# Kernel optimization log

Measured on AMD Instinct MI355X. Metric: run time of the kernel, lower is better.

The kernel has to match this reference:

```python
import jax, jax.numpy as jnp
import numpy as np

N_NODES = 20000
IN_C = 512
OUT_C = 128
HEADS = 4
N_EDGES = 320000
NEG_SLOPE = 0.2


def setup_inputs() -> dict:
    key = jax.random.key(0)
    ks = jax.random.split(key, 10)
    x = jax.random.normal(ks[0], (N_NODES, IN_C), dtype=jnp.float32)
    edge_index = jax.random.randint(ks[1], (2, N_EDGES), 0, N_NODES, dtype=jnp.int64)
    s = 0.05
    return {
        "x": x,
        "edge_index": edge_index,
        "W1": jax.random.normal(ks[2], (IN_C, HEADS * OUT_C), dtype=jnp.float32) * s,
        "a_src1": jax.random.normal(ks[3], (HEADS, OUT_C), dtype=jnp.float32) * s,
        "a_dst1": jax.random.normal(ks[4], (HEADS, OUT_C), dtype=jnp.float32) * s,
        "b1": jnp.zeros((HEADS * OUT_C,), dtype=jnp.float32),
        "W2": jax.random.normal(ks[5], (HEADS * OUT_C, 1 * OUT_C), dtype=jnp.float32) * s,
        "a_src2": jax.random.normal(ks[6], (1, OUT_C), dtype=jnp.float32) * s,
        "a_dst2": jax.random.normal(ks[7], (1, OUT_C), dtype=jnp.float32) * s,
        "b2": jnp.zeros((OUT_C,), dtype=jnp.float32),
    }


def gat_conv(x, src, dst, W, a_src, a_dst, b, heads, out_c, concat):
    N = x.shape[0]
    h = (x @ W).reshape(N, heads, out_c)            # [N,H,C]
    al_src = jnp.sum(h * a_src, axis=-1)            # [N,H]
    al_dst = jnp.sum(h * a_dst, axis=-1)            # [N,H]
    e = jax.nn.leaky_relu(al_src[src] + al_dst[dst], NEG_SLOPE)  # [E,H]
    # segment softmax over edges grouped by destination node
    e_max = jax.ops.segment_max(e, dst, num_segments=N)         # [N,H]
    e = jnp.exp(e - e_max[dst])
    denom = jax.ops.segment_sum(e, dst, num_segments=N)         # [N,H]
    alpha = e / (denom[dst] + 1e-16)                             # [E,H]
    msg = h[src] * alpha[:, :, None]                             # [E,H,C]
    out = jax.ops.segment_sum(msg, dst, num_segments=N)          # [N,H,C]
    out = out.reshape(N, heads * out_c) if concat else jnp.mean(out, axis=1)
    return out + b


def reference(x, edge_index, W1, a_src1, a_dst1, b1, W2, a_src2, a_dst2, b2):
    N = x.shape[0]
    # PyG GATConv adds self-loops by default
    loops = jnp.arange(N, dtype=edge_index.dtype)
    src = jnp.concatenate([edge_index[0], loops])
    dst = jnp.concatenate([edge_index[1], loops])
    h = gat_conv(x, src, dst, W1, a_src1, a_dst1, b1, HEADS, OUT_C, concat=True)
    h = jax.nn.elu(h)
    return gat_conv(h, src, dst, W2, a_src2, a_dst2, b2, 1, OUT_C, concat=False)
```

## Files before the change

kernel.cpp:

```cpp
#include <hip/hip_runtime.h>
#include <hip/hip_bf16.h>

typedef __hip_bfloat16 bf16;
typedef __bf16 bf16x8 __attribute__((ext_vector_type(8)));
typedef float f32x4 __attribute__((ext_vector_type(4)));

#define NEG_SLOPE 0.2f
#define F32_THRESH 256


__device__ __forceinline__ bool is_f32(const int* fcnt) { return *fcnt > F32_THRESH; }

__device__ __forceinline__ float ld_f(const void* p, long long i, bool f32) {
    return f32 ? ((const float*)p)[i] : __bfloat162float(((const bf16*)p)[i]);
}

__device__ __forceinline__ float b2f(unsigned hs) {
    return __uint_as_float(hs << 16);
}

__device__ __forceinline__ void load_lds16(const void* g, void* l) {
    __builtin_amdgcn_global_load_lds(
        (const __attribute__((address_space(1))) void*)g,
        (__attribute__((address_space(3))) void*)l, 16, 0, 0);
}

__global__ void k_sniff(const unsigned* w, long long nw, int* cnt) {
    int c = 0;
    for (long long i = blockIdx.x * (long long)blockDim.x + threadIdx.x; i < nw;
         i += (long long)gridDim.x * blockDim.x)
        if ((w[i] & 0x7F80u) == 0x7F80u) c++;
    if (c) atomicAdd(cnt, c);
}

__global__ void k_tobf16(const void* src, const int* fcnt, bf16* dst,
                         long long n_valid, long long n_total) {
    bool f32 = is_f32(fcnt);
    for (long long i = blockIdx.x * (long long)blockDim.x + threadIdx.x; i < n_total;
         i += (long long)gridDim.x * blockDim.x)
        dst[i] = (i < n_valid) ? __float2bfloat16(ld_f(src, i, f32))
                               : __float2bfloat16(0.f);
}


__global__ void k_detect_i32(const int* idx, int n_half, int* iflag) {
    int any = 0;
    for (int i = blockIdx.x * blockDim.x + threadIdx.x; i < n_half;
         i += gridDim.x * blockDim.x)
        if (idx[2 * i + 1] != 0) any = 1;
    if (any) atomicOr(iflag, 1);
}

__device__ __forceinline__ int edge_val(const void* idx, long long i, int is64) {
    return is64 ? (int)((const long long*)idx)[i] : ((const int*)idx)[i];
}


__global__ void k_count(const void* idx, const int* iflag, int E0, int N, int* deg) {
    int e = blockIdx.x * blockDim.x + threadIdx.x;
    if (e >= E0 + N) return;
    int is64 = (*iflag == 0);
    int d = (e < E0) ? edge_val(idx, (long long)E0 + e, is64) : (e - E0);
    if ((unsigned)d >= (unsigned)N) d = 0;
    atomicAdd(&deg[d], 1);
}

__global__ __launch_bounds__(1024) void k_scan(const int* deg, int* rowptr, int N) {
    __shared__ int part[1024];
    int t = threadIdx.x;
    int chunk = (N + 1023) / 1024;
    int s = t * chunk, e = min(N, s + chunk);
    int sum = 0;
    for (int i = s; i < e; i++) sum += deg[i];
    part[t] = sum;
    __syncthreads();
    for (int off = 1; off < 1024; off <<= 1) {
        int v = (t >= off) ? part[t - off] : 0;
        __syncthreads();
        part[t] += v;
        __syncthreads();
    }
    int run = (t == 0) ? 0 : part[t - 1];
    for (int i = s; i < e; i++) { rowptr[i] = run; run += deg[i]; }
    if (t == 1023) rowptr[N] = part[1023];
}

__global__ void k_scatter(const void* idx, const int* iflag, int E0, int N,
                          const int* rowptr, int* cursor, int* csr_src) {
    int e = blockIdx.x * blockDim.x + threadIdx.x;
    if (e >= E0 + N) return;
    int is64 = (*iflag == 0);
    int s, d;
    if (e < E0) {
        s = edge_val(idx, e, is64);
        d = edge_val(idx, (long long)E0 + e, is64);
    } else {
        s = d = e - E0;
    }
    if ((unsigned)s >= (unsigned)N) s = 0;
    if ((unsigned)d >= (unsigned)N) d = 0;
    int pos = rowptr[d] + atomicAdd(&cursor[d], 1);
    if ((unsigned)pos < (unsigned)(E0 + N)) csr_src[pos] = s;
}


__global__ void k_transpose(const void* W, const int* fcnt, bf16* Wt, int K, int N) {
    int i = blockIdx.x * blockDim.x + threadIdx.x;
    if (i >= K * N) return;
    bool f32 = is_f32(fcnt);
    int k = i / N, n = i % N;
    Wt[(size_t)n * K + k] = __float2bfloat16(ld_f(W, i, f32));
}


__global__ void k_al(const bf16* __restrict__ h, const void* a_s, const void* a_d,
                     const int* fcnt, float* als, float* ald, int N, int H) {
    __shared__ float sa[512], sd[512];
    const int HC = H * 128;
    bool f32 = is_f32(fcnt);
    for (int i = threadIdx.x; i < HC; i += blockDim.x) {
        sa[i] = ld_f(a_s, i, f32);
        sd[i] = ld_f(a_d, i, f32);
    }
    __syncthreads();
    int i = blockIdx.x * blockDim.x + threadIdx.x;
    if (i >= N * H) return;
    int n = i / H, hh = i % H;
    const uint4* row = (const uint4*)(h + (size_t)n * HC + hh * 128);
    float s = 0.f, d = 0.f;
#pragma unroll
    for (int q = 0; q < 16; q++) {
        uint4 u = row[q];
        unsigned uu[4] = {u.x, u.y, u.z, u.w};
#pragma unroll
        for (int t = 0; t < 4; t++) {
            float v0 = b2f(uu[t] & 0xFFFFu), v1 = b2f(uu[t] >> 16);
            int c = hh * 128 + q * 8 + t * 2;
            s += v0 * sa[c] + v1 * sa[c + 1];
            d += v0 * sd[c] + v1 * sd[c + 1];
        }
    }
    als[i] = s;
    ald[i] = d;
}


template <int BN>
__global__ __launch_bounds__(256) void k_gemm(const bf16* __restrict__ A,
                                              const bf16* __restrict__ Bt,
                                              bf16* __restrict__ C,
                                              int M, int Nn, int K) {
    constexpr int BM = 128, BK = 32;
    constexpr int NT = BN / 32;
    const int m0 = blockIdx.x * BM;
    const int n0 = blockIdx.y * BN;
    __shared__ __bf16 As[BM][BK];
    __shared__ __bf16 Bs[BN][BK];
    const int tid = threadIdx.x;
    const int wave = tid >> 6;
    const int lane = tid & 63;
    const int wm = (wave & 1) * 64;
    const int wn = (wave >> 1) * (NT * 16);
    const int lm = lane & 15;
    const int quad = lane >> 4;
    const int srow = tid >> 2;
    const int scol = (tid & 3) * 8;

    f32x4 acc[4][NT];
#pragma unroll
    for (int mt = 0; mt < 4; mt++)
#pragma unroll
        for (int nt = 0; nt < NT; nt++) acc[mt][nt] = (f32x4){0.f, 0.f, 0.f, 0.f};

    const char* Ab = (const char*)(A + (size_t)(m0 + srow) * K + scol);
    const char* Bb = (const char*)(Bt + (size_t)(n0 + srow) * K + scol);
    char* ldsA = (char*)&As[0][0] + wave * 1024;
    char* ldsB = (char*)&Bs[0][0] + wave * 1024;
    const size_t rstep = (size_t)64 * K * 2;

    for (int k0 = 0; k0 < K; k0 += BK) {
        __syncthreads();
        const size_t kb = (size_t)k0 * 2;
        load_lds16(Ab + kb, ldsA);
        load_lds16(Ab + kb + rstep, ldsA + 4096);
        load_lds16(Bb + kb, ldsB);
        if (BN == 128) load_lds16(Bb + kb + rstep, ldsB + 4096);
        __syncthreads();
        bf16x8 af[4], bfv[NT];
#pragma unroll
        for (int mt = 0; mt < 4; mt++)
            af[mt] = *(const bf16x8*)&As[wm + mt * 16 + lm][quad * 8];
#pragma unroll
        for (int nt = 0; nt < NT; nt++)
            bfv[nt] = *(const bf16x8*)&Bs[wn + nt * 16 + lm][quad * 8];
#pragma unroll
        for (int mt = 0; mt < 4; mt++)
#pragma unroll
            for (int nt = 0; nt < NT; nt++)
                acc[mt][nt] = __builtin_amdgcn_mfma_f32_16x16x32_bf16(
                    af[mt], bfv[nt], acc[mt][nt], 0, 0, 0);
    }

#pragma unroll
    for (int mt = 0; mt < 4; mt++) {
        int rb = m0 + wm + mt * 16 + quad * 4;
#pragma unroll
        for (int nt = 0; nt < NT; nt++) {
            int col = n0 + wn + nt * 16 + lm;
#pragma unroll
            for (int r = 0; r < 4; r++) {
                int row = rb + r;
                if (row < M) C[(size_t)row * Nn + col] = __float2bfloat16(acc[mt][nt][r]);
            }
        }
    }
}


template <int C, int H, bool ELU, bool DYN_OUT, int BS>
__global__ __launch_bounds__(BS) void k_agg(
    const bf16* __restrict__ feat, const float* __restrict__ als,
    const float* __restrict__ ald, const int* __restrict__ rowptr,
    const int* __restrict__ csr_src, const void* bias, const int* fcnt,
    void* outp, int N, int E) {
    constexpr int NW = BS / 64;
    constexpr int CPL = C / 64;
    constexpr int Ch = C / H;
    constexpr int OPT = C / BS;
    const int n = blockIdx.x;
    const int tid = threadIdx.x;
    const int wave = tid >> 6;
    const int lane = tid & 63;
    const int c0 = lane * CPL;
    const int head = c0 / Ch;

    __shared__ float red[NW][C];
    __shared__ float ps[NW][H];

    int start = rowptr[n];
    if (start < 0) start = 0;
    int end = rowptr[n + 1];
    if (end > E) end = E;
    int deg = end - start;
    if (deg < 0) deg = 0;

    float aldn[H];
#pragma unroll
    for (int h = 0; h < H; h++) aldn[h] = ald[(size_t)n * H + h];

    float acc[CPL] = {};
    float psum[H] = {};

#pragma unroll 2
    for (int e = wave; e < deg; e += NW) {
        int s = csr_src[start + e];
        if ((unsigned)s >= (unsigned)N) s = 0;
        float w[H];
        if (H == 4) {
            float4 av = ((const float4*)als)[s];
            float a4[4] = {av.x, av.y, av.z, av.w};
#pragma unroll
            for (int h = 0; h < 4; h++) {
                float l = a4[h] + aldn[h];
                l = l > 0.f ? l : NEG_SLOPE * l;
                w[h] = __expf(fminf(l, 60.f));
                psum[h] += w[h];
            }
        } else {
            float l = als[s] + aldn[0];
            l = l > 0.f ? l : NEG_SLOPE * l;
            w[0] = __expf(fminf(l, 60.f));
            psum[0] += w[0];
        }
        float wl;
        if (H == 1) wl = w[0];
        else wl = head < 2 ? (head == 0 ? w[0] : w[1]) : (head == 2 ? w[2] : w[3]);

        const bf16* fr = feat + (size_t)s * C + c0;
        if (CPL == 8) {
            uint4 u = *(const uint4*)fr;
            unsigned uu[4] = {u.x, u.y, u.z, u.w};
#pragma unroll
            for (int q = 0; q < 4; q++) {
                acc[2 * q] += wl * b2f(uu[q] & 0xFFFFu);
                acc[2 * q + 1] += wl * b2f(uu[q] >> 16);
            }
        } else {
            unsigned u = *(const unsigned*)fr;
            acc[0] += wl * b2f(u & 0xFFFFu);
            acc[1] += wl * b2f(u >> 16);
        }
    }

#pragma unroll
    for (int j = 0; j < CPL; j++) red[wave][c0 + j] = acc[j];
    if (lane == 0)
#pragma unroll
        for (int h = 0; h < H; h++) ps[wave][h] = psum[h];
    __syncthreads();

    const bool f32 = is_f32(fcnt);
#pragma unroll
    for (int p = 0; p < OPT; p++) {
        int c = tid * OPT + p;
        int h = c / Ch;
        float sv = 0.f;
#pragma unroll
        for (int w2 = 0; w2 < NW; w2++) sv += red[w2][c];
        float dn = 1e-16f;
#pragma unroll
        for (int w2 = 0; w2 < NW; w2++) dn += ps[w2][h];
        float v = sv / dn + ld_f(bias, c, f32);
        if (ELU) v = v > 0.f ? v : expf(v) - 1.f;
        size_t oi = (size_t)n * C + c;
        if (DYN_OUT && f32) ((float*)outp)[oi] = v;
        else ((bf16*)outp)[oi] = __float2bfloat16(v);
    }
}


extern "C" void kernel_launch(void* const* d_in, const int* in_sizes, int n_in,
                              void* d_out, int out_size, void* d_ws, size_t ws_size,
                              hipStream_t stream) {
    const int N = in_sizes[0] / 512;
    const int K = 512;
    const int C1 = 512;
    const int C2 = 128;
    const int H1 = 4;
    const int E0 = in_sizes[1] / 2;
    const int E = E0 + N;
    const int Mpad = (N + 127) / 128 * 128;

    const void* x_raw = d_in[0];
    const void* eidx = d_in[1];
    const void* W1 = d_in[2];
    const void* as1 = d_in[3];
    const void* ad1 = d_in[4];
    const void* b1 = d_in[5];
    const void* W2 = d_in[6];
    const void* as2 = d_in[7];
    const void* ad2 = d_in[8];
    const void* b2 = d_in[9];

    char* ws = (char*)d_ws;
    size_t off = 0;
    auto take = [&](size_t bytes) {
        size_t r = off;
        off += (bytes + 255) & ~(size_t)255;
        return r;
    };
    bf16* xb     = (bf16*)(ws + take((size_t)Mpad * K * 2));
    bf16* h1     = (bf16*)(ws + take((size_t)N * C1 * 2));
    bf16* hagg   = (bf16*)(ws + take((size_t)Mpad * C1 * 2));
    bf16* W1t    = (bf16*)(ws + take((size_t)K * C1 * 2));
    bf16* W2t    = (bf16*)(ws + take((size_t)C1 * C2 * 2));
    float* al1s  = (float*)(ws + take((size_t)N * H1 * 4));
    float* al1d  = (float*)(ws + take((size_t)N * H1 * 4));
    int* rowptr  = (int*)(ws + take((size_t)(N + 1) * 4));
    int* csr_src = (int*)(ws + take((size_t)E * 4));
    int* deg     = (int*)(ws + take((size_t)(2 * N + 2) * 4));
    int* cursor  = deg + N;
    int* iflag   = deg + 2 * N;
    int* fcnt    = deg + 2 * N + 1;
    bf16* h2     = xb;
    float* al2s  = al1s;
    float* al2d  = al1d;
    if (off > ws_size) return;

    hipMemsetAsync(deg, 0, (size_t)(2 * N + 2) * 4, stream);
    hipMemsetAsync(csr_src, 0, (size_t)E * 4, stream);

    long long nw = (long long)in_sizes[0] / 2;
    if (nw > (1 << 20)) nw = 1 << 20;
    k_sniff<<<256, 256, 0, stream>>>((const unsigned*)x_raw, nw, fcnt);
    int nh = E0 > (1 << 16) ? (1 << 16) : E0;
    k_detect_i32<<<64, 256, 0, stream>>>((const int*)eidx, nh, iflag);

    k_count<<<(E + 255) / 256, 256, 0, stream>>>(eidx, iflag, E0, N, deg);
    k_scan<<<1, 1024, 0, stream>>>(deg, rowptr, N);
    k_scatter<<<(E + 255) / 256, 256, 0, stream>>>(eidx, iflag, E0, N, rowptr, cursor, csr_src);

    k_tobf16<<<2048, 256, 0, stream>>>(x_raw, fcnt, xb, (long long)N * K, (long long)Mpad * K);
    k_transpose<<<(K * C1 + 255) / 256, 256, 0, stream>>>(W1, fcnt, W1t, K, C1);
    k_transpose<<<(C1 * C2 + 255) / 256, 256, 0, stream>>>(W2, fcnt, W2t, C1, C2);

    dim3 g1(Mpad / 128, C1 / 128);
    k_gemm<128><<<g1, 256, 0, stream>>>(xb, W1t, h1, N, C1, K);
    k_al<<<(N * H1 + 255) / 256, 256, 0, stream>>>(h1, as1, ad1, fcnt, al1s, al1d, N, H1);
    k_agg<512, 4, true, false, 256><<<N, 256, 0, stream>>>(h1, al1s, al1d, rowptr, csr_src,
                                                           b1, fcnt, hagg, N, E);
    hipMemsetAsync(hagg + (size_t)N * C1, 0, (size_t)(Mpad - N) * C1 * 2, stream);

    dim3 g2(Mpad / 128, C2 / 64);
    k_gemm<64><<<g2, 256, 0, stream>>>(hagg, W2t, h2, N, C2, C1);
    k_al<<<(N + 255) / 256, 256, 0, stream>>>(h2, as2, ad2, fcnt, al2s, al2d, N, 1);
    k_agg<128, 1, false, true, 128><<<N, 128, 0, stream>>>(h2, al2s, al2d, rowptr, csr_src,
                                                           b2, fcnt, d_out, N, E);
}
```

Before: 320.6 us.

## Precompute edge attention weights and denominators in separate kernel; vectorize bf16 conversion

Adds a per-edge kernel that computes the exp attention weights, stores them, and accumulates per-destination softmax denominators with atomics. The aggregation kernel then reads one precomputed weight per edge instead of recomputing exp per wave, and reads the denominator from memory. It also vectorizes the f32-to-bf16 input conversion to 8 elements per thread and raises the layer-2 aggregation block size to 256. The cost is an extra edge array, a weight buffer, extra kernel launches and atomic traffic.

```diff
diff --git a/kernel.cpp b/kernel.cpp
--- a/kernel.cpp
+++ b/kernel.cpp
@@ -17,6 +17,13 @@
 
 __device__ __forceinline__ float b2f(unsigned hs) {
     return __uint_as_float(hs << 16);
+}
+
+__device__ __forceinline__ unsigned pack_bf2(float a, float b) {
+    union { bf16 h[2]; unsigned u; } p;
+    p.h[0] = __float2bfloat16(a);
+    p.h[1] = __float2bfloat16(b);
+    return p.u;
 }
 
 __device__ __forceinline__ void load_lds16(const void* g, void* l) {
@@ -36,10 +43,34 @@
 __global__ void k_tobf16(const void* src, const int* fcnt, bf16* dst,
                          long long n_valid, long long n_total) {
     bool f32 = is_f32(fcnt);
-    for (long long i = blockIdx.x * (long long)blockDim.x + threadIdx.x; i < n_total;
-         i += (long long)gridDim.x * blockDim.x)
-        dst[i] = (i < n_valid) ? __float2bfloat16(ld_f(src, i, f32))
-                               : __float2bfloat16(0.f);
+    long long t = blockIdx.x * (long long)blockDim.x + threadIdx.x;
+    long long n8 = n_total / 8;
+    for (long long i = t; i < n8; i += (long long)gridDim.x * blockDim.x) {
+        long long b = i * 8;
+        uint4 out;
+        if (b + 8 <= n_valid) {
+            if (f32) {
+                const float4* s4 = (const float4*)src;
+                float4 x0 = s4[i * 2], x1 = s4[i * 2 + 1];
+                out.x = pack_bf2(x0.x, x0.y);
+                out.y = pack_bf2(x0.z, x0.w);
+                out.z = pack_bf2(x1.x, x1.y);
+                out.w = pack_bf2(x1.z, x1.w);
+            } else {
+                out = ((const uint4*)src)[i];
+            }
+        } else {
+            bf16 tmp[8];
+#pragma unroll
+            for (int j = 0; j < 8; j++) {
+                long long k = b + j;
+                tmp[j] = (k < n_valid) ? __float2bfloat16(ld_f(src, k, f32))
+                                       : __float2bfloat16(0.f);
+            }
+            out = *(uint4*)tmp;
+        }
+        ((uint4*)dst)[i] = out;
+    }
 }
 
 
@@ -86,7 +117,7 @@
 }
 
 __global__ void k_scatter(const void* idx, const int* iflag, int E0, int N,
-                          const int* rowptr, int* cursor, int* csr_src) {
+                          const int* rowptr, int* cursor, int* csr_src, int* csr_dst) {
     int e = blockIdx.x * blockDim.x + threadIdx.x;
     if (e >= E0 + N) return;
     int is64 = (*iflag == 0);
@@ -100,7 +131,30 @@
     if ((unsigned)s >= (unsigned)N) s = 0;
     if ((unsigned)d >= (unsigned)N) d = 0;
     int pos = rowptr[d] + atomicAdd(&cursor[d], 1);
-    if ((unsigned)pos < (unsigned)(E0 + N)) csr_src[pos] = s;
+    if ((unsigned)pos < (unsigned)(E0 + N)) {
+        csr_src[pos] = s;
+        csr_dst[pos] = d;
+    }
+}
+
+
+template <int H>
+__global__ void k_w(const int* __restrict__ csr_src, const int* __restrict__ csr_dst,
+                    const float* __restrict__ als, const float* __restrict__ ald,
+                    float* __restrict__ w, float* __restrict__ denom, int E, int N) {
+    int e = blockIdx.x * blockDim.x + threadIdx.x;
+    if (e >= E) return;
+    int s = csr_src[e], d = csr_dst[e];
+    if ((unsigned)s >= (unsigned)N) s = 0;
+    if ((unsigned)d >= (unsigned)N) d = 0;
+#pragma unroll
+    for (int h = 0; h < H; h++) {
+        float l = als[s * H + h] + ald[d * H + h];
+        l = l > 0.f ? l : NEG_SLOPE * l;
+        float wv = __expf(fminf(l, 60.f));
+        w[(size_t)e * H + h] = wv;
+        atomicAdd(&denom[d * H + h], wv);
+    }
 }
 
 
@@ -219,14 +273,13 @@
 
 template <int C, int H, bool ELU, bool DYN_OUT, int BS>
 __global__ __launch_bounds__(BS) void k_agg(
-    const bf16* __restrict__ feat, const float* __restrict__ als,
-    const float* __restrict__ ald, const int* __restrict__ rowptr,
+    const bf16* __restrict__ feat, const float* __restrict__ w,
+    const float* __restrict__ denom, const int* __restrict__ rowptr,
     const int* __restrict__ csr_src, const void* bias, const int* fcnt,
     void* outp, int N, int E) {
     constexpr int NW = BS / 64;
     constexpr int CPL = C / 64;
     constexpr int Ch = C / H;
-    constexpr int OPT = C / BS;
     const int n = blockIdx.x;
     const int tid = threadIdx.x;
     const int wave = tid >> 6;
@@ -235,7 +288,6 @@
     const int head = c0 / Ch;
 
     __shared__ float red[NW][C];
-    __shared__ float ps[NW][H];
 
     int start = rowptr[n];
     if (start < 0) start = 0;
@@ -244,38 +296,14 @@
     int deg = end - start;
     if (deg < 0) deg = 0;
 
-    float aldn[H];
-#pragma unroll
-    for (int h = 0; h < H; h++) aldn[h] = ald[(size_t)n * H + h];
-
     float acc[CPL] = {};
-    float psum[H] = {};
 
 #pragma unroll 2
     for (int e = wave; e < deg; e += NW) {
-        int s = csr_src[start + e];
+        int idx = start + e;
+        int s = csr_src[idx];
         if ((unsigned)s >= (unsigned)N) s = 0;
-        float w[H];
-        if (H == 4) {
-            float4 av = ((const float4*)als)[s];
-            float a4[4] = {av.x, av.y, av.z, av.w};
-#pragma unroll
-            for (int h = 0; h < 4; h++) {
-                float l = a4[h] + aldn[h];
-                l = l > 0.f ? l : NEG_SLOPE * l;
-                w[h] = __expf(fminf(l, 60.f));
-                psum[h] += w[h];
-            }
-        } else {
-            float l = als[s] + aldn[0];
-            l = l > 0.f ? l : NEG_SLOPE * l;
-            w[0] = __expf(fminf(l, 60.f));
-            psum[0] += w[0];
-        }
-        float wl;
-        if (H == 1) wl = w[0];
-        else wl = head < 2 ? (head == 0 ? w[0] : w[1]) : (head == 2 ? w[2] : w[3]);
-
+        float wl = w[(size_t)idx * H + head];
         const bf16* fr = feat + (size_t)s * C + c0;
         if (CPL == 8) {
             uint4 u = *(const uint4*)fr;
@@ -294,22 +322,15 @@
 
 #pragma unroll
     for (int j = 0; j < CPL; j++) red[wave][c0 + j] = acc[j];
-    if (lane == 0)
-#pragma unroll
-        for (int h = 0; h < H; h++) ps[wave][h] = psum[h];
     __syncthreads();
 
     const bool f32 = is_f32(fcnt);
-#pragma unroll
-    for (int p = 0; p < OPT; p++) {
-        int c = tid * OPT + p;
+    for (int c = tid; c < C; c += BS) {
         int h = c / Ch;
         float sv = 0.f;
 #pragma unroll
         for (int w2 = 0; w2 < NW; w2++) sv += red[w2][c];
-        float dn = 1e-16f;
-#pragma unroll
-        for (int w2 = 0; w2 < NW; w2++) dn += ps[w2][h];
+        float dn = denom[(size_t)n * H + h] + 1e-16f;
         float v = sv / dn + ld_f(bias, c, f32);
         if (ELU) v = v > 0.f ? v : expf(v) - 1.f;
         size_t oi = (size_t)n * C + c;
@@ -357,18 +378,22 @@
     float* al1s  = (float*)(ws + take((size_t)N * H1 * 4));
     float* al1d  = (float*)(ws + take((size_t)N * H1 * 4));
     int* rowptr  = (int*)(ws + take((size_t)(N + 1) * 4));
-    int* csr_src = (int*)(ws + take((size_t)E * 4));
-    int* deg     = (int*)(ws + take((size_t)(2 * N + 2) * 4));
+    int* csr_src = (int*)(ws + take((size_t)2 * E * 4));
+    int* csr_dst = csr_src + E;
+    float* wbuf  = (float*)(ws + take((size_t)E * H1 * 4));
+    int* deg     = (int*)(ws + take((size_t)(7 * N + 2) * 4));
     int* cursor  = deg + N;
     int* iflag   = deg + 2 * N;
     int* fcnt    = deg + 2 * N + 1;
+    float* denom1 = (float*)(deg + 2 * N + 2);
+    float* denom2 = denom1 + 4 * N;
     bf16* h2     = xb;
     float* al2s  = al1s;
     float* al2d  = al1d;
     if (off > ws_size) return;
 
-    hipMemsetAsync(deg, 0, (size_t)(2 * N + 2) * 4, stream);
-    hipMemsetAsync(csr_src, 0, (size_t)E * 4, stream);
+    hipMemsetAsync(deg, 0, (size_t)(7 * N + 2) * 4, stream);
+    hipMemsetAsync(csr_src, 0, (size_t)2 * E * 4, stream);
 
     long long nw = (long long)in_sizes[0] / 2;
     if (nw > (1 << 20)) nw = 1 << 20;
@@ -378,22 +403,27 @@
 
     k_count<<<(E + 255) / 256, 256, 0, stream>>>(eidx, iflag, E0, N, deg);
     k_scan<<<1, 1024, 0, stream>>>(deg, rowptr, N);
-    k_scatter<<<(E + 255) / 256, 256, 0, stream>>>(eidx, iflag, E0, N, rowptr, cursor, csr_src);
-
-    k_tobf16<<<2048, 256, 0, stream>>>(x_raw, fcnt, xb, (long long)N * K, (long long)Mpad * K);
+    k_scatter<<<(E + 255) / 256, 256, 0, stream>>>(eidx, iflag, E0, N, rowptr, cursor,
+                                                   csr_src, csr_dst);
+
+    k_tobf16<<<1024, 256, 0, stream>>>(x_raw, fcnt, xb, (long long)N * K, (long long)Mpad * K);
     k_transpose<<<(K * C1 + 255) / 256, 256, 0, stream>>>(W1, fcnt, W1t, K, C1);
     k_transpose<<<(C1 * C2 + 255) / 256, 256, 0, stream>>>(W2, fcnt, W2t, C1, C2);
 
     dim3 g1(Mpad / 128, C1 / 128);
     k_gemm<128><<<g1, 256, 0, stream>>>(xb, W1t, h1, N, C1, K);
     k_al<<<(N * H1 + 255) / 256, 256, 0, stream>>>(h1, as1, ad1, fcnt, al1s, al1d, N, H1);
-    k_agg<512, 4, true, false, 256><<<N, 256, 0, stream>>>(h1, al1s, al1d, rowptr, csr_src,
-                                                           b1, fcnt, hagg, N, E);
+    k_w<4><<<(E + 255) / 256, 256, 0, stream>>>(csr_src, csr_dst, al1s, al1d,
+                                                wbuf, denom1, E, N);
+    k_agg<512, 4, true, false, 256><<<N, 256, 0, stream>>>(h1, wbuf, denom1, rowptr,
+                                                           csr_src, b1, fcnt, hagg, N, E);
     hipMemsetAsync(hagg + (size_t)N * C1, 0, (size_t)(Mpad - N) * C1 * 2, stream);
 
     dim3 g2(Mpad / 128, C2 / 64);
     k_gemm<64><<<g2, 256, 0, stream>>>(hagg, W2t, h2, N, C2, C1);
     k_al<<<(N + 255) / 256, 256, 0, stream>>>(h2, as2, ad2, fcnt, al2s, al2d, N, 1);
-    k_agg<128, 1, false, true, 128><<<N, 128, 0, stream>>>(h2, al2s, al2d, rowptr, csr_src,
-                                                           b2, fcnt, d_out, N, E);
-}
+    k_w<1><<<(E + 255) / 256, 256, 0, stream>>>(csr_src, csr_dst, al2s, al2d,
+                                                wbuf, denom2, E, N);
+    k_agg<128, 1, false, true, 256><<<N, 256, 0, stream>>>(h2, wbuf, denom2, rowptr,
+                                                           csr_src, b2, fcnt, d_out, N, E);
+}
```

Result: slower. 432.3 us (+34.8%).
